# Performance work log

Hardware: AMD Instinct MI355X
Metric: run time of the kernel (lower is better)

The kernel has to match this reference:

```python
import jax, jax.numpy as jnp
import numpy as np

D_MODEL = 1024
N_HEADS = 16
HEAD_DIM = D_MODEL // N_HEADS


def setup_inputs() -> dict:
    key = jax.random.key(0)
    ks = jax.random.split(key, 5)
    B, T = 4, 2048
    x = jax.random.normal(ks[0], (B, T, D_MODEL), dtype=jnp.float32)
    s = 0.02
    W_qkv = jax.random.normal(ks[1], (D_MODEL, 3 * D_MODEL), dtype=jnp.float32) * s
    b_qkv = jnp.zeros((3 * D_MODEL,), dtype=jnp.float32)
    W_out = jax.random.normal(ks[2], (D_MODEL, D_MODEL), dtype=jnp.float32) * s
    b_out = jnp.zeros((D_MODEL,), dtype=jnp.float32)
    return {"x": x, "W_qkv": W_qkv, "b_qkv": b_qkv, "W_out": W_out, "b_out": b_out}


def reference(x, W_qkv, b_qkv, W_out, b_out):
    B, T, C = x.shape
    H, Dh = N_HEADS, HEAD_DIM
    qkv = x @ W_qkv + b_qkv                      # [B,T,3C]
    q, k, v = jnp.split(qkv, 3, axis=-1)
    q = q.reshape(B, T, H, Dh).transpose(0, 2, 1, 3)  # [B,H,T,Dh]
    k = k.reshape(B, T, H, Dh).transpose(0, 2, 1, 3)
    v = v.reshape(B, T, H, Dh).transpose(0, 2, 1, 3)
    scale = 1.0 / jnp.sqrt(jnp.float32(Dh))
    scores = jnp.einsum('bhqd,bhkd->bhqk', q, k) * scale  # [B,H,T,T]
    causal = jnp.tril(jnp.ones((T, T), dtype=bool))
    scores = jnp.where(causal[None, None], scores, jnp.float32(-jnp.inf))
    w = jax.nn.softmax(scores, axis=-1)
    y = jnp.einsum('bhqk,bhkd->bhqd', w, v)      # [B,H,T,Dh]
    y = y.transpose(0, 2, 1, 3).reshape(B, T, C)
    return y @ W_out + b_out
```

## Files before the change

kernel.cpp:

```cpp
#include <hip/hip_runtime.h>
#include <cstdint>
#include <math.h>

#define TT 2048
#define CC 1024
#define HH 16
#define DH 64
#define BB 4
#define MM 8192

typedef unsigned short u16;
typedef __bf16 bf16_t;
typedef bf16_t bf16x8 __attribute__((ext_vector_type(8)));
typedef float f32x4 __attribute__((ext_vector_type(4)));

static __device__ inline u16 f2bf(float f) {
    unsigned int u = __builtin_bit_cast(unsigned int, f);
    unsigned int lsb = (u >> 16) & 1u;
    u += 0x7fffu + lsb;
    return (u16)(u >> 16);
}

static __device__ inline unsigned int cvt_pk_bf16(float a, float b) {
    unsigned int r;
    asm volatile("v_cvt_pk_bf16_f32 %0, %1, %2" : "=v"(r) : "v"(a), "v"(b));
    return r;
}

#define GLL16(gptr, lptr)                                                            \
    __builtin_amdgcn_global_load_lds(                                                \
        (__attribute__((address_space(1))) void*)(gptr),                             \
        (__attribute__((address_space(3))) void*)(lptr), 16, 0, 0)


__global__ void cast_x_kernel(const float* __restrict__ x, u16* __restrict__ xb, int n4) {
    int i = blockIdx.x * blockDim.x + threadIdx.x;
    if (i >= n4) return;
    float4 v = ((const float4*)x)[i];
    uint2 o;
    o.x = cvt_pk_bf16(v.x, v.y);
    o.y = cvt_pk_bf16(v.z, v.w);
    ((uint2*)xb)[i] = o;
}

__global__ void __launch_bounds__(256)
transpose_cast_kernel(const float* __restrict__ W, u16* __restrict__ Wt, int K, int N) {
    __shared__ u16 tile[32 * 34];
    const int tx = threadIdx.x & 31;
    const int ty = threadIdx.x >> 5;
    const int n0 = blockIdx.x * 32;
    const int k0 = blockIdx.y * 32;
#pragma unroll
    for (int i = 0; i < 4; ++i) {
        int k = ty + i * 8;
        tile[tx * 34 + k] = f2bf(W[(size_t)(k0 + k) * N + n0 + tx]);
    }
    __syncthreads();
    const int tx2 = threadIdx.x & 15;
    const int ty2 = threadIdx.x >> 4;
#pragma unroll
    for (int i = 0; i < 2; ++i) {
        int r = ty2 + i * 16;
        *(unsigned int*)&Wt[(size_t)(n0 + r) * K + k0 + 2 * tx2] =
            *(unsigned int*)&tile[r * 34 + 2 * tx2];
    }
}

template <int MODE>
__global__ void __launch_bounds__(256)
gemm_bt_kernel(const u16* __restrict__ A, const u16* __restrict__ Bt,
               const float* __restrict__ bias, float* __restrict__ Cout,
               u16* __restrict__ qws, u16* __restrict__ kws, u16* __restrict__ vtws,
               int Mdim, int Ndim, int Kdim) {
    __shared__ u16 As[2][128 * 32];
    __shared__ u16 Bs[2][128 * 32];

    const int tid  = threadIdx.x;
    const int w    = tid >> 6;
    const int lane = tid & 63;
    const int l15  = lane & 15;
    const int quad = lane >> 4;
    const int wm   = (w & 1) * 64;
    const int wn   = (w >> 1) * 64;
    const int m0   = blockIdx.y * 128;
    const int n0   = blockIdx.x * 128;

    const int row0  = tid >> 2;
    const int row1  = row0 + 64;
    const int col8  = (tid & 3) << 3;

    f32x4 acc[4][4];
#pragma unroll
    for (int i = 0; i < 4; ++i)
#pragma unroll
        for (int j = 0; j < 4; ++j) acc[i][j] = (f32x4){0.f, 0.f, 0.f, 0.f};

    auto stageA = [&](int buf, int kc) {
        if (MODE == 0) {
            int kcc = kc + col8, h = kcc >> 6, d = kcc & 63;
            int m = m0 + row0, b = m >> 11, t = m & 2047;
            GLL16(&A[(((size_t)(b * HH + h) * TT + t) * DH) + d], &As[buf][tid * 8]);
            m = m0 + row1; b = m >> 11; t = m & 2047;
            GLL16(&A[(((size_t)(b * HH + h) * TT + t) * DH) + d], &As[buf][(tid + 256) * 8]);
        } else {
            GLL16(&A[(size_t)(m0 + row0) * Kdim + kc + col8], &As[buf][tid * 8]);
            GLL16(&A[(size_t)(m0 + row1) * Kdim + kc + col8], &As[buf][(tid + 256) * 8]);
        }
    };

    stageA(0, 0);
    GLL16(&Bt[(size_t)(n0 + row0) * Kdim + col8], &Bs[0][tid * 8]);
    GLL16(&Bt[(size_t)(n0 + row1) * Kdim + col8], &Bs[0][(tid + 256) * 8]);

    const int nsteps = Kdim >> 5;
    for (int it = 0; it < nsteps; ++it) {
        const int buf = it & 1;
        __syncthreads();

        if (it + 1 < nsteps) {
            const int nbuf = buf ^ 1;
            const int kc = (it + 1) << 5;
            stageA(nbuf, kc);
            GLL16(&Bt[(size_t)(n0 + row0) * Kdim + kc + col8], &Bs[nbuf][tid * 8]);
            GLL16(&Bt[(size_t)(n0 + row1) * Kdim + kc + col8], &Bs[nbuf][(tid + 256) * 8]);
        }

        bf16x8 af[4], bfm[4];
#pragma unroll
        for (int mt = 0; mt < 4; ++mt)
            af[mt] = *(const bf16x8*)&As[buf][(wm + mt * 16 + l15) * 32 + quad * 8];
#pragma unroll
        for (int nt = 0; nt < 4; ++nt)
            bfm[nt] = *(const bf16x8*)&Bs[buf][(wn + nt * 16 + l15) * 32 + quad * 8];
#pragma unroll
        for (int mt = 0; mt < 4; ++mt)
#pragma unroll
            for (int nt = 0; nt < 4; ++nt)
                acc[mt][nt] = __builtin_amdgcn_mfma_f32_16x16x32_bf16(
                    af[mt], bfm[nt], acc[mt][nt], 0, 0, 0);
    }

#pragma unroll
    for (int mt = 0; mt < 4; ++mt) {
        int mrow_base = m0 + wm + mt * 16 + quad * 4;
#pragma unroll
        for (int nt = 0; nt < 4; ++nt) {
            int ncol = n0 + wn + nt * 16 + l15;
            float bv = bias[ncol];
            if (MODE == 0) {
#pragma unroll
                for (int r = 0; r < 4; ++r)
                    Cout[(size_t)(mrow_base + r) * Ndim + ncol] = acc[mt][nt][r] + bv;
            } else {
                int which = ncol >> 10, c = ncol & 1023;
                int h = c >> 6, d = c & 63;
                if (which == 2) {
                    int b = mrow_base >> 11, t = mrow_base & 2047;
                    int bh = b * HH + h;
                    uint2 pv;
                    pv.x = cvt_pk_bf16(acc[mt][nt][0] + bv, acc[mt][nt][1] + bv);
                    pv.y = cvt_pk_bf16(acc[mt][nt][2] + bv, acc[mt][nt][3] + bv);
                    *(uint2*)&vtws[((size_t)bh * DH + d) * TT + t] = pv;
                } else {
#pragma unroll
                    for (int r = 0; r < 4; ++r) {
                        int mrow = mrow_base + r;
                        int b = mrow >> 11, t = mrow & 2047;
                        int bh = b * HH + h;
                        float val = acc[mt][nt][r] + bv;
                        if (which == 0) {
                            qws[((size_t)bh * TT + t) * DH + d] = f2bf(val * 0.18033688f);
                        } else {
                            kws[((size_t)bh * TT + t) * DH + d] = f2bf(val);
                        }
                    }
                }
            }
        }
    }
}

__global__ void __launch_bounds__(512, 4)
attn_kernel(const u16* __restrict__ qws, const u16* __restrict__ kws,
            const u16* __restrict__ vtws, u16* __restrict__ yws) {
    __shared__ u16 Ks[2][64 * 68];
    __shared__ u16 Vs[2][64 * 68];
    __shared__ u16 Ps[8][16 * 68];

    const int tid  = threadIdx.x;
    const int w    = tid >> 6;
    const int lane = tid & 63;
    const int l15  = lane & 15;
    const int quad = lane >> 4;
    const int bh   = blockIdx.x;
    const int p    = blockIdx.y;

    const u16* Kbase = kws + (size_t)bh * TT * DH;
    const u16* Vbase = vtws + (size_t)bh * DH * TT;
    u16* Pw = &Ps[w][0];

    const int srow  = tid >> 3;
    const int scol8 = (tid & 7) << 3;

    bf16x8 aones;
#pragma unroll
    for (int i = 0; i < 8; ++i) aones[i] = __builtin_bit_cast(bf16_t, (u16)0x3F80);

#pragma unroll
    for (int phase = 0; phase < 2; ++phase) {
        const int qt     = phase == 0 ? (15 - p) : p;
        const int q0     = qt * 128;
        const int qr0    = q0 + w * 16;
        const int ntiles = (q0 + 128) >> 6;

        const u16* Qp = qws + ((size_t)bh * TT + qr0) * DH;
        bf16x8 bq[2];
#pragma unroll
        for (int kk = 0; kk < 2; ++kk)
            bq[kk] = *(const bf16x8*)&Qp[l15 * DH + kk * 32 + quad * 8];

        f32x4 o[4], ol;
#pragma unroll
        for (int dt = 0; dt < 4; ++dt) o[dt] = (f32x4){0.f, 0.f, 0.f, 0.f};
        ol = (f32x4){0.f, 0.f, 0.f, 0.f};

        uint4 pk = *(const uint4*)&Kbase[(size_t)srow * DH + scol8];
        uint4 pv = *(const uint4*)&Vbase[(size_t)srow * TT + scol8];
        __syncthreads();
        *(uint4*)&Ks[0][srow * 68 + scol8] = pk;
        *(uint4*)&Vs[0][srow * 68 + scol8] = pv;
        if (ntiles > 1) {
            pk = *(const uint4*)&Kbase[(size_t)(64 + srow) * DH + scol8];
            pv = *(const uint4*)&Vbase[(size_t)srow * TT + 64 + scol8];
        }

        for (int it = 0; it < ntiles; ++it) {
            const int buf = it & 1;
            __syncthreads();

            if (it + 1 < ntiles) {
                *(uint4*)&Ks[buf ^ 1][srow * 68 + scol8] = pk;
                *(uint4*)&Vs[buf ^ 1][srow * 68 + scol8] = pv;
                if (it + 2 < ntiles) {
                    int jn = (it + 2) << 6;
                    pk = *(const uint4*)&Kbase[(size_t)(jn + srow) * DH + scol8];
                    pv = *(const uint4*)&Vbase[(size_t)srow * TT + jn + scol8];
                }
            }

            const int j0 = it << 6;
            if (j0 > qr0 + 15) continue;

            f32x4 s[4];
#pragma unroll
            for (int kt = 0; kt < 4; ++kt) s[kt] = (f32x4){0.f, 0.f, 0.f, 0.f};
            __builtin_amdgcn_s_setprio(1);
#pragma unroll
            for (int kk = 0; kk < 2; ++kk)
#pragma unroll
                for (int kt = 0; kt < 4; ++kt) {
                    bf16x8 ak = *(const bf16x8*)&Ks[buf][(kt * 16 + l15) * 68 + kk * 32 + quad * 8];
                    s[kt] = __builtin_amdgcn_mfma_f32_16x16x32_bf16(ak, bq[kk], s[kt], 0, 0, 0);
                }
            __builtin_amdgcn_s_setprio(0);

            if (j0 + 63 > qr0) {
                int qy = qr0 + l15;
#pragma unroll
                for (int kt = 0; kt < 4; ++kt)
#pragma unroll
                    for (int r = 0; r < 4; ++r) {
                        int key = j0 + kt * 16 + quad * 4 + r;
                        if (key > qy) s[kt][r] = -INFINITY;
                    }
            }

#pragma unroll
            for (int kt = 0; kt < 4; ++kt)
#pragma unroll
                for (int r = 0; r < 4; ++r)
                    s[kt][r] = __builtin_amdgcn_exp2f(s[kt][r]);

            bf16x8 avr0[4];
#pragma unroll
            for (int dt = 0; dt < 4; ++dt)
                avr0[dt] = *(const bf16x8*)&Vs[buf][(dt * 16 + l15) * 68 + quad * 8];

#pragma unroll
            for (int kt = 0; kt < 4; ++kt) {
                uint2 pkd;
                pkd.x = cvt_pk_bf16(s[kt][0], s[kt][1]);
                pkd.y = cvt_pk_bf16(s[kt][2], s[kt][3]);
                *(uint2*)&Pw[l15 * 68 + kt * 16 + quad * 4] = pkd;
            }
            asm volatile("s_waitcnt lgkmcnt(0)" ::: "memory");

            bf16x8 bp0 = *(const bf16x8*)&Pw[l15 * 68 + quad * 8];
            bf16x8 bp1 = *(const bf16x8*)&Pw[l15 * 68 + 32 + quad * 8];
            bf16x8 avr1[4];
#pragma unroll
            for (int dt = 0; dt < 4; ++dt)
                avr1[dt] = *(const bf16x8*)&Vs[buf][(dt * 16 + l15) * 68 + 32 + quad * 8];

            __builtin_amdgcn_s_setprio(1);
#pragma unroll
            for (int dt = 0; dt < 4; ++dt)
                o[dt] = __builtin_amdgcn_mfma_f32_16x16x32_bf16(avr0[dt], bp0, o[dt], 0, 0, 0);
            ol = __builtin_amdgcn_mfma_f32_16x16x32_bf16(aones, bp0, ol, 0, 0, 0);
#pragma unroll
            for (int dt = 0; dt < 4; ++dt)
                o[dt] = __builtin_amdgcn_mfma_f32_16x16x32_bf16(avr1[dt], bp1, o[dt], 0, 0, 0);
            ol = __builtin_amdgcn_mfma_f32_16x16x32_bf16(aones, bp1, ol, 0, 0, 0);
            __builtin_amdgcn_s_setprio(0);
        }

        float rinv = __builtin_amdgcn_rcpf(ol[0]);
        int t = qr0 + l15;
#pragma unroll
        for (int dt = 0; dt < 4; ++dt) {
            uint2 yv;
            yv.x = cvt_pk_bf16(o[dt][0] * rinv, o[dt][1] * rinv);
            yv.y = cvt_pk_bf16(o[dt][2] * rinv, o[dt][3] * rinv);
            *(uint2*)&yws[((size_t)bh * TT + t) * DH + dt * 16 + quad * 4] = yv;
        }
    }
}


extern "C" void kernel_launch(void* const* d_in, const int* in_sizes, int n_in,
                              void* d_out, int out_size, void* d_ws, size_t ws_size,
                              hipStream_t stream) {
    const float* x     = (const float*)d_in[0];
    const float* W_qkv = (const float*)d_in[1];
    const float* b_qkv = (const float*)d_in[2];
    const float* W_out = (const float*)d_in[3];
    const float* b_out = (const float*)d_in[4];
    float* out = (float*)d_out;

    char* ws = (char*)d_ws;
    u16* xb   = (u16*)ws; ws += (size_t)MM * CC * 2;
    u16* wqt  = (u16*)ws; ws += (size_t)3 * CC * CC * 2;
    u16* wot  = (u16*)ws; ws += (size_t)CC * CC * 2;
    u16* qws  = (u16*)ws; ws += (size_t)MM * CC * 2;
    u16* kws  = (u16*)ws; ws += (size_t)MM * CC * 2;
    u16* vtws = (u16*)ws; ws += (size_t)MM * CC * 2;
    u16* yws  = (u16*)ws; ws += (size_t)MM * CC * 2;

    cast_x_kernel<<<(MM * CC / 4) / 256, 256, 0, stream>>>(x, xb, MM * CC / 4);
    transpose_cast_kernel<<<dim3(3 * CC / 32, CC / 32), 256, 0, stream>>>(W_qkv, wqt, CC, 3 * CC);
    transpose_cast_kernel<<<dim3(CC / 32, CC / 32), 256, 0, stream>>>(W_out, wot, CC, CC);

    gemm_bt_kernel<1><<<dim3(24, 64), 256, 0, stream>>>(
        xb, wqt, b_qkv, nullptr, qws, kws, vtws, MM, 3 * CC, CC);

    attn_kernel<<<dim3(BB * HH, 8), 512, 0, stream>>>(qws, kws, vtws, yws);

    gemm_bt_kernel<0><<<dim3(8, 64), 256, 0, stream>>>(
        yws, wot, b_out, out, nullptr, nullptr, nullptr, MM, CC, CC);
}
```

Before: 282.7 us.

## Give each attention wave 32 query rows, sharing K/V fragment loads across two groups

The attention block drops from 8 waves of 16 query rows to 4 waves of 32 query rows each. Each wave loads its K and V LDS fragments once and reuses them for two 16-row query groups, halving LDS reads per unit of MFMA work. The tile-staging loads are widened to 16 elements per thread to fit the smaller block. In exchange the block has half as many threads, register pressure per wave rises (launch bounds change to 256,3), the causal skip is coarser at 32-row granularity, and the setprio hints are removed.

New measurement: 274.8 us. 2.8% less time.

```diff
diff --git a/kernel.cpp b/kernel.cpp
--- a/kernel.cpp
+++ b/kernel.cpp
@@ -180,12 +180,12 @@
     }
 }
 
-__global__ void __launch_bounds__(512, 4)
+__global__ void __launch_bounds__(256, 3)
 attn_kernel(const u16* __restrict__ qws, const u16* __restrict__ kws,
             const u16* __restrict__ vtws, u16* __restrict__ yws) {
     __shared__ u16 Ks[2][64 * 68];
     __shared__ u16 Vs[2][64 * 68];
-    __shared__ u16 Ps[8][16 * 68];
+    __shared__ u16 Ps[4][32 * 68];
 
     const int tid  = threadIdx.x;
     const int w    = tid >> 6;
@@ -199,8 +199,8 @@
     const u16* Vbase = vtws + (size_t)bh * DH * TT;
     u16* Pw = &Ps[w][0];
 
-    const int srow  = tid >> 3;
-    const int scol8 = (tid & 7) << 3;
+    const int srow  = tid >> 2;
+    const int sc16  = (tid & 3) << 4;
 
     bf16x8 aones;
 #pragma unroll
@@ -210,28 +210,39 @@
     for (int phase = 0; phase < 2; ++phase) {
         const int qt     = phase == 0 ? (15 - p) : p;
         const int q0     = qt * 128;
-        const int qr0    = q0 + w * 16;
+        const int qr0    = q0 + w * 32;
         const int ntiles = (q0 + 128) >> 6;
 
         const u16* Qp = qws + ((size_t)bh * TT + qr0) * DH;
-        bf16x8 bq[2];
-#pragma unroll
-        for (int kk = 0; kk < 2; ++kk)
-            bq[kk] = *(const bf16x8*)&Qp[l15 * DH + kk * 32 + quad * 8];
-
-        f32x4 o[4], ol;
-#pragma unroll
-        for (int dt = 0; dt < 4; ++dt) o[dt] = (f32x4){0.f, 0.f, 0.f, 0.f};
-        ol = (f32x4){0.f, 0.f, 0.f, 0.f};
-
-        uint4 pk = *(const uint4*)&Kbase[(size_t)srow * DH + scol8];
-        uint4 pv = *(const uint4*)&Vbase[(size_t)srow * TT + scol8];
+        bf16x8 bqa[2], bqb[2];
+#pragma unroll
+        for (int kk = 0; kk < 2; ++kk) {
+            bqa[kk] = *(const bf16x8*)&Qp[l15 * DH + kk * 32 + quad * 8];
+            bqb[kk] = *(const bf16x8*)&Qp[(16 + l15) * DH + kk * 32 + quad * 8];
+        }
+
+        f32x4 o[2][4], ol[2];
+#pragma unroll
+        for (int qg = 0; qg < 2; ++qg) {
+#pragma unroll
+            for (int dt = 0; dt < 4; ++dt) o[qg][dt] = (f32x4){0.f, 0.f, 0.f, 0.f};
+            ol[qg] = (f32x4){0.f, 0.f, 0.f, 0.f};
+        }
+
+        uint4 pk0 = *(const uint4*)&Kbase[(size_t)srow * DH + sc16];
+        uint4 pk1 = *(const uint4*)&Kbase[(size_t)srow * DH + sc16 + 8];
+        uint4 pv0 = *(const uint4*)&Vbase[(size_t)srow * TT + sc16];
+        uint4 pv1 = *(const uint4*)&Vbase[(size_t)srow * TT + sc16 + 8];
         __syncthreads();
-        *(uint4*)&Ks[0][srow * 68 + scol8] = pk;
-        *(uint4*)&Vs[0][srow * 68 + scol8] = pv;
+        *(uint4*)&Ks[0][srow * 68 + sc16]     = pk0;
+        *(uint4*)&Ks[0][srow * 68 + sc16 + 8] = pk1;
+        *(uint4*)&Vs[0][srow * 68 + sc16]     = pv0;
+        *(uint4*)&Vs[0][srow * 68 + sc16 + 8] = pv1;
         if (ntiles > 1) {
-            pk = *(const uint4*)&Kbase[(size_t)(64 + srow) * DH + scol8];
-            pv = *(const uint4*)&Vbase[(size_t)srow * TT + 64 + scol8];
+            pk0 = *(const uint4*)&Kbase[(size_t)(64 + srow) * DH + sc16];
+            pk1 = *(const uint4*)&Kbase[(size_t)(64 + srow) * DH + sc16 + 8];
+            pv0 = *(const uint4*)&Vbase[(size_t)srow * TT + 64 + sc16];
+            pv1 = *(const uint4*)&Vbase[(size_t)srow * TT + 64 + sc16 + 8];
         }
 
         for (int it = 0; it < ntiles; ++it) {
@@ -239,89 +250,114 @@
             __syncthreads();
 
             if (it + 1 < ntiles) {
-                *(uint4*)&Ks[buf ^ 1][srow * 68 + scol8] = pk;
-                *(uint4*)&Vs[buf ^ 1][srow * 68 + scol8] = pv;
+                *(uint4*)&Ks[buf ^ 1][srow * 68 + sc16]     = pk0;
+                *(uint4*)&Ks[buf ^ 1][srow * 68 + sc16 + 8] = pk1;
+                *(uint4*)&Vs[buf ^ 1][srow * 68 + sc16]     = pv0;
+                *(uint4*)&Vs[buf ^ 1][srow * 68 + sc16 + 8] = pv1;
                 if (it + 2 < ntiles) {
                     int jn = (it + 2) << 6;
-                    pk = *(const uint4*)&Kbase[(size_t)(jn + srow) * DH + scol8];
-                    pv = *(const uint4*)&Vbase[(size_t)srow * TT + jn + scol8];
+                    pk0 = *(const uint4*)&Kbase[(size_t)(jn + srow) * DH + sc16];
+                    pk1 = *(const uint4*)&Kbase[(size_t)(jn + srow) * DH + sc16 + 8];
+                    pv0 = *(const uint4*)&Vbase[(size_t)srow * TT + jn + sc16];
+                    pv1 = *(const uint4*)&Vbase[(size_t)srow * TT + jn + sc16 + 8];
                 }
             }
 
             const int j0 = it << 6;
-            if (j0 > qr0 + 15) continue;
-
-            f32x4 s[4];
-#pragma unroll
-            for (int kt = 0; kt < 4; ++kt) s[kt] = (f32x4){0.f, 0.f, 0.f, 0.f};
-            __builtin_amdgcn_s_setprio(1);
+            if (j0 > qr0 + 31) continue;
+
+            bf16x8 ak[8];
 #pragma unroll
             for (int kk = 0; kk < 2; ++kk)
 #pragma unroll
-                for (int kt = 0; kt < 4; ++kt) {
-                    bf16x8 ak = *(const bf16x8*)&Ks[buf][(kt * 16 + l15) * 68 + kk * 32 + quad * 8];
-                    s[kt] = __builtin_amdgcn_mfma_f32_16x16x32_bf16(ak, bq[kk], s[kt], 0, 0, 0);
-                }
-            __builtin_amdgcn_s_setprio(0);
+                for (int kt = 0; kt < 4; ++kt)
+                    ak[kk * 4 + kt] =
+                        *(const bf16x8*)&Ks[buf][(kt * 16 + l15) * 68 + kk * 32 + quad * 8];
+
+            f32x4 sa[4], sb[4];
+#pragma unroll
+            for (int kt = 0; kt < 4; ++kt) {
+                sa[kt] = (f32x4){0.f, 0.f, 0.f, 0.f};
+                sb[kt] = (f32x4){0.f, 0.f, 0.f, 0.f};
+            }
+#pragma unroll
+            for (int kk = 0; kk < 2; ++kk)
+#pragma unroll
+                for (int kt = 0; kt < 4; ++kt)
+                    sa[kt] = __builtin_amdgcn_mfma_f32_16x16x32_bf16(ak[kk * 4 + kt], bqa[kk], sa[kt], 0, 0, 0);
+#pragma unroll
+            for (int kk = 0; kk < 2; ++kk)
+#pragma unroll
+                for (int kt = 0; kt < 4; ++kt)
+                    sb[kt] = __builtin_amdgcn_mfma_f32_16x16x32_bf16(ak[kk * 4 + kt], bqb[kk], sb[kt], 0, 0, 0);
 
             if (j0 + 63 > qr0) {
-                int qy = qr0 + l15;
+                int qy0 = qr0 + l15;
+                int qy1 = qr0 + 16 + l15;
 #pragma unroll
                 for (int kt = 0; kt < 4; ++kt)
 #pragma unroll
                     for (int r = 0; r < 4; ++r) {
                         int key = j0 + kt * 16 + quad * 4 + r;
-                        if (key > qy) s[kt][r] = -INFINITY;
+                        if (key > qy0) sa[kt][r] = -INFINITY;
+                        if (key > qy1) sb[kt][r] = -INFINITY;
                     }
             }
 
 #pragma unroll
             for (int kt = 0; kt < 4; ++kt)
 #pragma unroll
-                for (int r = 0; r < 4; ++r)
-                    s[kt][r] = __builtin_amdgcn_exp2f(s[kt][r]);
-
-            bf16x8 avr0[4];
-#pragma unroll
-            for (int dt = 0; dt < 4; ++dt)
-                avr0[dt] = *(const bf16x8*)&Vs[buf][(dt * 16 + l15) * 68 + quad * 8];
+                for (int r = 0; r < 4; ++r) {
+                    sa[kt][r] = __builtin_amdgcn_exp2f(sa[kt][r]);
+                    sb[kt][r] = __builtin_amdgcn_exp2f(sb[kt][r]);
+                }
+
+            bf16x8 avr[8];
+#pragma unroll
+            for (int kk = 0; kk < 2; ++kk)
+#pragma unroll
+                for (int dt = 0; dt < 4; ++dt)
+                    avr[kk * 4 + dt] =
+                        *(const bf16x8*)&Vs[buf][(dt * 16 + l15) * 68 + kk * 32 + quad * 8];
 
 #pragma unroll
             for (int kt = 0; kt < 4; ++kt) {
-                uint2 pkd;
-                pkd.x = cvt_pk_bf16(s[kt][0], s[kt][1]);
-                pkd.y = cvt_pk_bf16(s[kt][2], s[kt][3]);
-                *(uint2*)&Pw[l15 * 68 + kt * 16 + quad * 4] = pkd;
+                uint2 pda, pdb;
+                pda.x = cvt_pk_bf16(sa[kt][0], sa[kt][1]);
+                pda.y = cvt_pk_bf16(sa[kt][2], sa[kt][3]);
+                pdb.x = cvt_pk_bf16(sb[kt][0], sb[kt][1]);
+                pdb.y = cvt_pk_bf16(sb[kt][2], sb[kt][3]);
+                *(uint2*)&Pw[l15 * 68 + kt * 16 + quad * 4]        = pda;
+                *(uint2*)&Pw[(16 + l15) * 68 + kt * 16 + quad * 4] = pdb;
             }
             asm volatile("s_waitcnt lgkmcnt(0)" ::: "memory");
 
-            bf16x8 bp0 = *(const bf16x8*)&Pw[l15 * 68 + quad * 8];
-            bf16x8 bp1 = *(const bf16x8*)&Pw[l15 * 68 + 32 + quad * 8];
-            bf16x8 avr1[4];
-#pragma unroll
-            for (int dt = 0; dt < 4; ++dt)
-                avr1[dt] = *(const bf16x8*)&Vs[buf][(dt * 16 + l15) * 68 + 32 + quad * 8];
-
-            __builtin_amdgcn_s_setprio(1);
-#pragma unroll
-            for (int dt = 0; dt < 4; ++dt)
-                o[dt] = __builtin_amdgcn_mfma_f32_16x16x32_bf16(avr0[dt], bp0, o[dt], 0, 0, 0);
-            ol = __builtin_amdgcn_mfma_f32_16x16x32_bf16(aones, bp0, ol, 0, 0, 0);
-#pragma unroll
-            for (int dt = 0; dt < 4; ++dt)
-                o[dt] = __builtin_amdgcn_mfma_f32_16x16x32_bf16(avr1[dt], bp1, o[dt], 0, 0, 0);
-            ol = __builtin_amdgcn_mfma_f32_16x16x32_bf16(aones, bp1, ol, 0, 0, 0);
-            __builtin_amdgcn_s_setprio(0);
-        }
-
-        float rinv = __builtin_amdgcn_rcpf(ol[0]);
-        int t = qr0 + l15;
-#pragma unroll
-        for (int dt = 0; dt < 4; ++dt) {
-            uint2 yv;
-            yv.x = cvt_pk_bf16(o[dt][0] * rinv, o[dt][1] * rinv);
-            yv.y = cvt_pk_bf16(o[dt][2] * rinv, o[dt][3] * rinv);
-            *(uint2*)&yws[((size_t)bh * TT + t) * DH + dt * 16 + quad * 4] = yv;
+#pragma unroll
+            for (int qg = 0; qg < 2; ++qg) {
+                bf16x8 bp0 = *(const bf16x8*)&Pw[(qg * 16 + l15) * 68 + quad * 8];
+                bf16x8 bp1 = *(const bf16x8*)&Pw[(qg * 16 + l15) * 68 + 32 + quad * 8];
+#pragma unroll
+                for (int dt = 0; dt < 4; ++dt)
+                    o[qg][dt] = __builtin_amdgcn_mfma_f32_16x16x32_bf16(avr[dt], bp0, o[qg][dt], 0, 0, 0);
+                ol[qg] = __builtin_amdgcn_mfma_f32_16x16x32_bf16(aones, bp0, ol[qg], 0, 0, 0);
+#pragma unroll
+                for (int dt = 0; dt < 4; ++dt)
+                    o[qg][dt] = __builtin_amdgcn_mfma_f32_16x16x32_bf16(avr[4 + dt], bp1, o[qg][dt], 0, 0, 0);
+                ol[qg] = __builtin_amdgcn_mfma_f32_16x16x32_bf16(aones, bp1, ol[qg], 0, 0, 0);
+            }
+        }
+
+#pragma unroll
+        for (int qg = 0; qg < 2; ++qg) {
+            float rinv = __builtin_amdgcn_rcpf(ol[qg][0]);
+            int t = qr0 + qg * 16 + l15;
+#pragma unroll
+            for (int dt = 0; dt < 4; ++dt) {
+                uint2 yv;
+                yv.x = cvt_pk_bf16(o[qg][dt][0] * rinv, o[qg][dt][1] * rinv);
+                yv.y = cvt_pk_bf16(o[qg][dt][2] * rinv, o[qg][dt][3] * rinv);
+                *(uint2*)&yws[((size_t)bh * TT + t) * DH + dt * 16 + quad * 4] = yv;
+            }
         }
     }
 }
@@ -353,7 +389,7 @@
     gemm_bt_kernel<1><<<dim3(24, 64), 256, 0, stream>>>(
         xb, wqt, b_qkv, nullptr, qws, kws, vtws, MM, 3 * CC, CC);
 
-    attn_kernel<<<dim3(BB * HH, 8), 512, 0, stream>>>(qws, kws, vtws, yws);
+    attn_kernel<<<dim3(BB * HH, 8), 256, 0, stream>>>(qws, kws, vtws, yws);
 
     gemm_bt_kernel<0><<<dim3(8, 64), 256, 0, stream>>>(
         yws, wot, b_out, out, nullptr, nullptr, nullptr, MM, CC, CC);
```
